# Performance work log

Measured on AMD Instinct MI355X. Metric: run time of the kernel, lower is better.

The kernel has to match this reference:

```python
import jax, jax.numpy as jnp
import numpy as np

N, D, K, MAX_ITER = 131072, 64, 512, 5


def setup_inputs() -> dict:
    key = jax.random.key(0)
    k1, k2, k3 = jax.random.split(key, 3)
    X = jax.random.normal(k1, (N, D), dtype=jnp.float32)
    centers = jax.random.normal(k2, (K, D), dtype=jnp.float32)
    repl_idx = jax.random.randint(k3, (MAX_ITER, K), 0, N, dtype=jnp.int32)
    return {"X": X, "centers": centers, "repl_idx": repl_idx}


def _assign(X, centers):
    # squared euclidean distance matrix [N, K]; argmin identical to cdist argmin
    x2 = jnp.sum(X * X, axis=1, keepdims=True)          # [N,1]
    c2 = jnp.sum(centers * centers, axis=1)             # [K]
    d2 = x2 + c2[None, :] - 2.0 * (X @ centers.T)       # [N,K]
    return jnp.argmin(d2, axis=1)


def reference(X, centers, repl_idx):
    n_clusters = centers.shape[0]
    assignments = None
    for i in range(MAX_ITER):
        assignments = _assign(X, centers)
        # scatter_mean: per-cluster sum / count (empty clusters -> 0, as torch_scatter)
        sums = jax.ops.segment_sum(X, assignments, num_segments=n_clusters)
        counts = jax.ops.segment_sum(jnp.ones((X.shape[0],), X.dtype), assignments,
                                     num_segments=n_clusters)
        new_centers = sums / jnp.maximum(counts, 1.0)[:, None]
        # re-initialize any exactly-zero entries from random data points
        new_centers_init = X[repl_idx[i]]                 # [K,D]
        new_centers = jnp.where(new_centers == 0, new_centers_init, new_centers)
        centers = new_centers
    return assignments, centers
```

## Files before the change

kernel.cpp:

```cpp
#include <hip/hip_runtime.h>

#define N_PTS 131072
#define KC    512
#define DIM   64
#define MAXIT 5
#define NCHUNK 64
#define CHUNK_PTS (N_PTS / NCHUNK)
#define FIXSCALE 1099511627776.0

typedef short v8s __attribute__((ext_vector_type(8)));
typedef float v4f __attribute__((ext_vector_type(4)));

__device__ __forceinline__ unsigned short bf16_rtne(float x) {
    unsigned int u = __float_as_uint(x);
    return (unsigned short)((u + 0x7FFFu + ((u >> 16) & 1u)) >> 16);
}
__device__ __forceinline__ float bf16_f32(unsigned short b) {
    return __uint_as_float(((unsigned int)b) << 16);
}
__device__ __forceinline__ void split3(float x, short& h, short& m, short& l) {
    unsigned short hb = bf16_rtne(x);
    float r1 = x - bf16_f32(hb);
    unsigned short mb = bf16_rtne(r1);
    float r2 = r1 - bf16_f32(mb);
    h = (short)hb; m = (short)mb; l = (short)bf16_rtne(r2);
}

__global__ __launch_bounds__(256) void prep_kernel(
        const float* __restrict__ C, float* __restrict__ c2out,
        unsigned short* __restrict__ Ch, unsigned short* __restrict__ Cm,
        unsigned short* __restrict__ Cl) {
    int k = blockIdx.x * 256 + threadIdx.x;
    if (k < KC) {
        float sq[DIM];
        #pragma unroll
        for (int j = 0; j < DIM; ++j) {
            float c = C[k * DIM + j];
            sq[j] = c * c;
            short h, m, l;
            split3(c, h, m, l);
            Ch[k * DIM + j] = (unsigned short)h;
            Cm[k * DIM + j] = (unsigned short)m;
            Cl[k * DIM + j] = (unsigned short)l;
        }
        #pragma unroll
        for (int st = 1; st < DIM; st <<= 1)
            #pragma unroll
            for (int j = 0; j < DIM; j += 2 * st)
                sq[j] = sq[j] + sq[j + st];
        c2out[k] = sq[0];
    }
}

__global__ __launch_bounds__(256, 4) void assign_kernel(
        const float* __restrict__ X,
        const unsigned short* __restrict__ Ch,
        const unsigned short* __restrict__ Cm,
        const unsigned short* __restrict__ Cl,
        const float* __restrict__ c2v, float* __restrict__ out_f) {
    __shared__ short Bt[6 * 64 * 8];
    __shared__ float c2t[KC];
    __shared__ float x2p[4][2][16][8];
    __shared__ float x2f[4][2][16];

    const int t   = threadIdx.x;
    const int wv  = t >> 6;
    const int l   = t & 63;
    const int row = l & 15;
    const int q   = l >> 4;
    const int pbase = blockIdx.x * 128 + wv * 32;

    for (int i = t; i < KC; i += 256) c2t[i] = c2v[i];

    v8s ah[2][2], am[2][2], al[2][2];
    #pragma unroll
    for (int T = 0; T < 2; ++T) {
        const float* xr = X + (size_t)(pbase + T * 16 + row) * DIM + q * 8;
        #pragma unroll
        for (int kc = 0; kc < 2; ++kc) {
            float4 v0 = *(const float4*)(xr + kc * 32);
            float4 v1 = *(const float4*)(xr + kc * 32 + 4);
            float e[8] = { v0.x, v0.y, v0.z, v0.w, v1.x, v1.y, v1.z, v1.w };
            v8s H, M, L;
            #pragma unroll
            for (int j = 0; j < 8; ++j) {
                short hh, mm, ll;
                split3(e[j], hh, mm, ll);
                H[j] = hh; M[j] = mm; L[j] = ll;
            }
            ah[T][kc] = H; am[T][kc] = M; al[T][kc] = L;
            float s0 = e[0]*e[0], s1 = e[1]*e[1], s2 = e[2]*e[2], s3 = e[3]*e[3];
            float s4 = e[4]*e[4], s5 = e[5]*e[5], s6 = e[6]*e[6], s7 = e[7]*e[7];
            x2p[wv][T][row][kc * 4 + q] =
                ((s0 + s1) + (s2 + s3)) + ((s4 + s5) + (s6 + s7));
        }
    }
    __syncthreads();
    if (t < 128) {
        int w2 = t >> 5, T2 = (t >> 4) & 1, pt = t & 15;
        const float* P = x2p[w2][T2][pt];
        x2f[w2][T2][pt] = ((P[0] + P[1]) + (P[2] + P[3]))
                        + ((P[4] + P[5]) + (P[6] + P[7]));
    }
    __syncthreads();
    float x2x[2][4];
    #pragma unroll
    for (int T = 0; T < 2; ++T)
        #pragma unroll
        for (int r = 0; r < 4; ++r)
            x2x[T][r] = x2f[wv][T][q * 4 + r];

    float bd[2][4];
    int   bk[2][4];
    #pragma unroll
    for (int T = 0; T < 2; ++T)
        #pragma unroll
        for (int r = 0; r < 4; ++r) { bd[T][r] = 3.4e38f; bk[T][r] = 0; }

    const unsigned short* const bases[3] = { Ch, Cm, Cl };
    #define CHUNK_GPTR(c, ct) ((const v8s*)(bases[(c) >> 7] +                 \
        ((size_t)((ct) * 16 + (((c) & 63) & 15)) * 64 +                       \
         (((c) >> 6) & 1) * 32 + (((c) & 63) >> 4) * 8)))

    v8s r1 = *CHUNK_GPTR(t, 0);
    v8s r2;
    if (t < 128) r2 = *CHUNK_GPTR(256 + t, 0);

    v8s* const BtV = (v8s*)Bt;
    for (int ct = 0; ct < 32; ++ct) {
        __syncthreads();
        BtV[t] = r1;
        if (t < 128) BtV[256 + t] = r2;
        if (ct < 31) {
            r1 = *CHUNK_GPTR(t, ct + 1);
            if (t < 128) r2 = *CHUNK_GPTR(256 + t, ct + 1);
        }
        __syncthreads();

        v8s bh0 = BtV[0 * 64 + l];
        v8s bh1 = BtV[1 * 64 + l];
        v8s bm0 = BtV[2 * 64 + l];
        v8s bm1 = BtV[3 * 64 + l];
        v8s bl0 = BtV[4 * 64 + l];
        v8s bl1 = BtV[5 * 64 + l];
        float c2k = c2t[ct * 16 + row];

        #pragma unroll
        for (int T = 0; T < 2; ++T) {
            v4f acc = {0.f, 0.f, 0.f, 0.f};
            acc = __builtin_amdgcn_mfma_f32_16x16x32_bf16(ah[T][0], bh0, acc, 0, 0, 0);
            acc = __builtin_amdgcn_mfma_f32_16x16x32_bf16(ah[T][1], bh1, acc, 0, 0, 0);
            acc = __builtin_amdgcn_mfma_f32_16x16x32_bf16(am[T][0], bh0, acc, 0, 0, 0);
            acc = __builtin_amdgcn_mfma_f32_16x16x32_bf16(am[T][1], bh1, acc, 0, 0, 0);
            acc = __builtin_amdgcn_mfma_f32_16x16x32_bf16(ah[T][0], bm0, acc, 0, 0, 0);
            acc = __builtin_amdgcn_mfma_f32_16x16x32_bf16(ah[T][1], bm1, acc, 0, 0, 0);
            acc = __builtin_amdgcn_mfma_f32_16x16x32_bf16(am[T][0], bm0, acc, 0, 0, 0);
            acc = __builtin_amdgcn_mfma_f32_16x16x32_bf16(am[T][1], bm1, acc, 0, 0, 0);
            acc = __builtin_amdgcn_mfma_f32_16x16x32_bf16(al[T][0], bh0, acc, 0, 0, 0);
            acc = __builtin_amdgcn_mfma_f32_16x16x32_bf16(al[T][1], bh1, acc, 0, 0, 0);
            acc = __builtin_amdgcn_mfma_f32_16x16x32_bf16(ah[T][0], bl0, acc, 0, 0, 0);
            acc = __builtin_amdgcn_mfma_f32_16x16x32_bf16(ah[T][1], bl1, acc, 0, 0, 0);
            #pragma unroll
            for (int r = 0; r < 4; ++r) {
                float tt = x2x[T][r] + c2k;
                float d2 = fmaf(-2.0f, acc[r], tt);
                if (d2 < bd[T][r]) { bd[T][r] = d2; bk[T][r] = ct * 16 + row; }
            }
        }
    }
    #undef CHUNK_GPTR

    #pragma unroll
    for (int T = 0; T < 2; ++T)
        #pragma unroll
        for (int r = 0; r < 4; ++r) {
            unsigned int b = __float_as_uint(bd[T][r]);
            b = (b & 0x80000000u) ? ~b : (b | 0x80000000u);
            unsigned long long key = ((unsigned long long)b << 32)
                                   | (unsigned int)bk[T][r];
            #pragma unroll
            for (int st = 1; st <= 8; st <<= 1) {
                unsigned long long o = __shfl_xor(key, st, 64);
                if (o < key) key = o;
            }
            if (row == 0) {
                int p = pbase + T * 16 + q * 4 + r;
                out_f[p] = (float)((int)(unsigned int)key);
            }
        }
}

__global__ __launch_bounds__(256) void accum_kernel(
        const float* __restrict__ X, const float* __restrict__ af,
        unsigned long long* __restrict__ qsums, int* __restrict__ counts) {
    __shared__ unsigned long long lsum[KC * 16];
    __shared__ int lcnt[KC];
    int slice = blockIdx.x & 3;
    int chunk = blockIdx.x >> 2;
    int p4 = threadIdx.x >> 2;
    int c4 = threadIdx.x & 3;

    for (int i = threadIdx.x; i < KC * 16; i += 256) lsum[i] = 0ull;
    for (int i = threadIdx.x; i < KC; i += 256) lcnt[i] = 0;
    __syncthreads();

    int base = chunk * CHUNK_PTS;
    #pragma unroll 2
    for (int it = 0; it < CHUNK_PTS / 64; ++it) {
        int n = base + it * 64 + p4;
        int a = (int)af[n];
        float4 xv = *(const float4*)(X + (size_t)n * DIM + slice * 16 + c4 * 4);
        long long q0 = (long long)llrint((double)xv.x * FIXSCALE);
        long long q1 = (long long)llrint((double)xv.y * FIXSCALE);
        long long q2 = (long long)llrint((double)xv.z * FIXSCALE);
        long long q3 = (long long)llrint((double)xv.w * FIXSCALE);
        atomicAdd(&lsum[a * 16 + c4 * 4 + 0], (unsigned long long)q0);
        atomicAdd(&lsum[a * 16 + c4 * 4 + 1], (unsigned long long)q1);
        atomicAdd(&lsum[a * 16 + c4 * 4 + 2], (unsigned long long)q2);
        atomicAdd(&lsum[a * 16 + c4 * 4 + 3], (unsigned long long)q3);
        if (slice == 0 && c4 == 0) atomicAdd(&lcnt[a], 1);
    }
    __syncthreads();

    for (int i = threadIdx.x; i < KC * 16; i += 256) {
        unsigned long long v = lsum[i];
        if (v != 0ull)
            atomicAdd(&qsums[(i >> 4) * DIM + slice * 16 + (i & 15)], v);
    }
    if (slice == 0)
        for (int i = threadIdx.x; i < KC; i += 256) {
            int v = lcnt[i];
            if (v != 0) atomicAdd(&counts[i], v);
        }
}

__global__ __launch_bounds__(256) void update_kernel(
        const unsigned long long* __restrict__ qsums,
        const int* __restrict__ counts,
        const int* __restrict__ repl, const float* __restrict__ X,
        float* __restrict__ outC, float* __restrict__ c2v,
        unsigned short* __restrict__ Ch, unsigned short* __restrict__ Cm,
        unsigned short* __restrict__ Cl) {
    int k = blockIdx.x * 4 + (threadIdx.x >> 6);
    int d = threadIdx.x & 63;

    long long qq = (long long)qsums[k * DIM + d];
    float s = (float)((double)qq * (1.0 / FIXSCALE));
    float cnt = (float)counts[k];
    float v = s / fmaxf(cnt, 1.0f);
    if (v == 0.0f) v = X[(size_t)repl[k] * DIM + d];
    outC[k * DIM + d] = v;

    short h, m, l;
    split3(v, h, m, l);
    Ch[k * DIM + d] = (unsigned short)h;
    Cm[k * DIM + d] = (unsigned short)m;
    Cl[k * DIM + d] = (unsigned short)l;

    float sq = v * v;
    #pragma unroll
    for (int st = 1; st < 64; st <<= 1)
        sq += __shfl_xor(sq, st, 64);
    if (d == 0) c2v[k] = sq;
}

extern "C" void kernel_launch(void* const* d_in, const int* in_sizes, int n_in,
                              void* d_out, int out_size, void* d_ws, size_t ws_size,
                              hipStream_t stream) {
    const float* X    = (const float*)d_in[0];
    const float* C0   = (const float*)d_in[1];
    const int*   repl = (const int*)d_in[2];
    float* out = (float*)d_out;

    char* ws = (char*)d_ws;
    unsigned short* Ch = (unsigned short*)(ws + 0);
    unsigned short* Cm = (unsigned short*)(ws + (64 << 10));
    unsigned short* Cl = (unsigned short*)(ws + (128 << 10));
    unsigned long long* qsums = (unsigned long long*)(ws + (192 << 10));
    int*   counts = (int*)  (ws + (448 << 10));
    float* c2v    = (float*)(ws + (450 << 10));

    prep_kernel<<<2, 256, 0, stream>>>(C0, c2v, Ch, Cm, Cl);

    for (int i = 0; i < MAXIT; ++i) {
        assign_kernel<<<N_PTS / 128, 256, 0, stream>>>(
            X, Ch, Cm, Cl, c2v, out);

        hipMemsetAsync(qsums, 0, KC * DIM * sizeof(unsigned long long)
                                 + KC * sizeof(int), stream);

        accum_kernel<<<NCHUNK * 4, 256, 0, stream>>>(X, out, qsums, counts);

        update_kernel<<<KC / 4, 256, 0, stream>>>(
            qsums, counts, repl + i * KC, X, out + N_PTS, c2v, Ch, Cm, Cl);
    }
}
```

Measured before the change: 474.6 us.

## Stage 64 centers per sync in assign, drop memset, widen accum blocks

The assign kernel now stages 64 centers (all three bf16 planes) into shared memory per barrier pair instead of 16, which cuts the number of barriers and global prefetch rounds. The trade is a larger LDS tile, more prefetch registers and an occupancy hint lowered from 4 to 3 blocks. The per-iteration hipMemsetAsync is removed: prep zeroes the sums and counts once, and update_kernel clears them after reading. accum_kernel now runs 1024-thread blocks so each block's shared-memory histogram serves more threads.

```diff
diff --git a/kernel.cpp b/kernel.cpp
--- a/kernel.cpp
+++ b/kernel.cpp
@@ -29,7 +29,8 @@
 __global__ __launch_bounds__(256) void prep_kernel(
         const float* __restrict__ C, float* __restrict__ c2out,
         unsigned short* __restrict__ Ch, unsigned short* __restrict__ Cm,
-        unsigned short* __restrict__ Cl) {
+        unsigned short* __restrict__ Cl,
+        unsigned long long* __restrict__ qsums, int* __restrict__ counts) {
     int k = blockIdx.x * 256 + threadIdx.x;
     if (k < KC) {
         float sq[DIM];
@@ -50,15 +51,18 @@
                 sq[j] = sq[j] + sq[j + st];
         c2out[k] = sq[0];
     }
-}
-
-__global__ __launch_bounds__(256, 4) void assign_kernel(
+    int t = blockIdx.x * 256 + threadIdx.x;
+    for (int i = t; i < KC * DIM; i += 512) qsums[i] = 0ull;
+    if (t < KC) counts[t] = 0;
+}
+
+__global__ __launch_bounds__(256, 3) void assign_kernel(
         const float* __restrict__ X,
         const unsigned short* __restrict__ Ch,
         const unsigned short* __restrict__ Cm,
         const unsigned short* __restrict__ Cl,
         const float* __restrict__ c2v, float* __restrict__ out_f) {
-    __shared__ short Bt[6 * 64 * 8];
+    __shared__ short Bt[1536 * 8];
     __shared__ float c2t[KC];
     __shared__ float x2p[4][2][16][8];
     __shared__ float x2f[4][2][16];
@@ -118,53 +122,57 @@
         for (int r = 0; r < 4; ++r) { bd[T][r] = 3.4e38f; bk[T][r] = 0; }
 
     const unsigned short* const bases[3] = { Ch, Cm, Cl };
-    #define CHUNK_GPTR(c, ct) ((const v8s*)(bases[(c) >> 7] +                 \
-        ((size_t)((ct) * 16 + (((c) & 63) & 15)) * 64 +                       \
-         (((c) >> 6) & 1) * 32 + (((c) & 63) >> 4) * 8)))
-
-    v8s r1 = *CHUNK_GPTR(t, 0);
-    v8s r2;
-    if (t < 128) r2 = *CHUNK_GPTR(256 + t, 0);
+    #define CHUNK_GPTR(c, s) ((const v8s*)(bases[((c) % 384) >> 7] +          \
+        ((size_t)((s) * 64 + ((c) / 384) * 16 + ((c) & 15)) * 64 +            \
+         ((((c) % 384) >> 6) & 1) * 32 + (((c) & 63) >> 4) * 8)))
+
+    v8s rr[6];
+    #pragma unroll
+    for (int r = 0; r < 6; ++r) rr[r] = *CHUNK_GPTR(t + 256 * r, 0);
 
     v8s* const BtV = (v8s*)Bt;
-    for (int ct = 0; ct < 32; ++ct) {
+    for (int s = 0; s < 8; ++s) {
         __syncthreads();
-        BtV[t] = r1;
-        if (t < 128) BtV[256 + t] = r2;
-        if (ct < 31) {
-            r1 = *CHUNK_GPTR(t, ct + 1);
-            if (t < 128) r2 = *CHUNK_GPTR(256 + t, ct + 1);
+        #pragma unroll
+        for (int r = 0; r < 6; ++r) BtV[t + 256 * r] = rr[r];
+        if (s < 7) {
+            #pragma unroll
+            for (int r = 0; r < 6; ++r) rr[r] = *CHUNK_GPTR(t + 256 * r, s + 1);
         }
         __syncthreads();
 
-        v8s bh0 = BtV[0 * 64 + l];
-        v8s bh1 = BtV[1 * 64 + l];
-        v8s bm0 = BtV[2 * 64 + l];
-        v8s bm1 = BtV[3 * 64 + l];
-        v8s bl0 = BtV[4 * 64 + l];
-        v8s bl1 = BtV[5 * 64 + l];
-        float c2k = c2t[ct * 16 + row];
-
-        #pragma unroll
-        for (int T = 0; T < 2; ++T) {
-            v4f acc = {0.f, 0.f, 0.f, 0.f};
-            acc = __builtin_amdgcn_mfma_f32_16x16x32_bf16(ah[T][0], bh0, acc, 0, 0, 0);
-            acc = __builtin_amdgcn_mfma_f32_16x16x32_bf16(ah[T][1], bh1, acc, 0, 0, 0);
-            acc = __builtin_amdgcn_mfma_f32_16x16x32_bf16(am[T][0], bh0, acc, 0, 0, 0);
-            acc = __builtin_amdgcn_mfma_f32_16x16x32_bf16(am[T][1], bh1, acc, 0, 0, 0);
-            acc = __builtin_amdgcn_mfma_f32_16x16x32_bf16(ah[T][0], bm0, acc, 0, 0, 0);
-            acc = __builtin_amdgcn_mfma_f32_16x16x32_bf16(ah[T][1], bm1, acc, 0, 0, 0);
-            acc = __builtin_amdgcn_mfma_f32_16x16x32_bf16(am[T][0], bm0, acc, 0, 0, 0);
-            acc = __builtin_amdgcn_mfma_f32_16x16x32_bf16(am[T][1], bm1, acc, 0, 0, 0);
-            acc = __builtin_amdgcn_mfma_f32_16x16x32_bf16(al[T][0], bh0, acc, 0, 0, 0);
-            acc = __builtin_amdgcn_mfma_f32_16x16x32_bf16(al[T][1], bh1, acc, 0, 0, 0);
-            acc = __builtin_amdgcn_mfma_f32_16x16x32_bf16(ah[T][0], bl0, acc, 0, 0, 0);
-            acc = __builtin_amdgcn_mfma_f32_16x16x32_bf16(ah[T][1], bl1, acc, 0, 0, 0);
-            #pragma unroll
-            for (int r = 0; r < 4; ++r) {
-                float tt = x2x[T][r] + c2k;
-                float d2 = fmaf(-2.0f, acc[r], tt);
-                if (d2 < bd[T][r]) { bd[T][r] = d2; bk[T][r] = ct * 16 + row; }
+        #pragma unroll
+        for (int sub = 0; sub < 4; ++sub) {
+            v8s bh0 = BtV[sub * 384 + 0 * 64 + l];
+            v8s bh1 = BtV[sub * 384 + 1 * 64 + l];
+            v8s bm0 = BtV[sub * 384 + 2 * 64 + l];
+            v8s bm1 = BtV[sub * 384 + 3 * 64 + l];
+            v8s bl0 = BtV[sub * 384 + 4 * 64 + l];
+            v8s bl1 = BtV[sub * 384 + 5 * 64 + l];
+            float c2k = c2t[s * 64 + sub * 16 + row];
+            int   kk  = s * 64 + sub * 16 + row;
+
+            #pragma unroll
+            for (int T = 0; T < 2; ++T) {
+                v4f acc = {0.f, 0.f, 0.f, 0.f};
+                acc = __builtin_amdgcn_mfma_f32_16x16x32_bf16(ah[T][0], bh0, acc, 0, 0, 0);
+                acc = __builtin_amdgcn_mfma_f32_16x16x32_bf16(ah[T][1], bh1, acc, 0, 0, 0);
+                acc = __builtin_amdgcn_mfma_f32_16x16x32_bf16(am[T][0], bh0, acc, 0, 0, 0);
+                acc = __builtin_amdgcn_mfma_f32_16x16x32_bf16(am[T][1], bh1, acc, 0, 0, 0);
+                acc = __builtin_amdgcn_mfma_f32_16x16x32_bf16(ah[T][0], bm0, acc, 0, 0, 0);
+                acc = __builtin_amdgcn_mfma_f32_16x16x32_bf16(ah[T][1], bm1, acc, 0, 0, 0);
+                acc = __builtin_amdgcn_mfma_f32_16x16x32_bf16(am[T][0], bm0, acc, 0, 0, 0);
+                acc = __builtin_amdgcn_mfma_f32_16x16x32_bf16(am[T][1], bm1, acc, 0, 0, 0);
+                acc = __builtin_amdgcn_mfma_f32_16x16x32_bf16(al[T][0], bh0, acc, 0, 0, 0);
+                acc = __builtin_amdgcn_mfma_f32_16x16x32_bf16(al[T][1], bh1, acc, 0, 0, 0);
+                acc = __builtin_amdgcn_mfma_f32_16x16x32_bf16(ah[T][0], bl0, acc, 0, 0, 0);
+                acc = __builtin_amdgcn_mfma_f32_16x16x32_bf16(ah[T][1], bl1, acc, 0, 0, 0);
+                #pragma unroll
+                for (int r = 0; r < 4; ++r) {
+                    float tt = x2x[T][r] + c2k;
+                    float d2 = fmaf(-2.0f, acc[r], tt);
+                    if (d2 < bd[T][r]) { bd[T][r] = d2; bk[T][r] = kk; }
+                }
             }
         }
     }
@@ -190,7 +198,7 @@
         }
 }
 
-__global__ __launch_bounds__(256) void accum_kernel(
+__global__ __launch_bounds__(1024) void accum_kernel(
         const float* __restrict__ X, const float* __restrict__ af,
         unsigned long long* __restrict__ qsums, int* __restrict__ counts) {
     __shared__ unsigned long long lsum[KC * 16];
@@ -200,14 +208,14 @@
     int p4 = threadIdx.x >> 2;
     int c4 = threadIdx.x & 3;
 
-    for (int i = threadIdx.x; i < KC * 16; i += 256) lsum[i] = 0ull;
-    for (int i = threadIdx.x; i < KC; i += 256) lcnt[i] = 0;
+    for (int i = threadIdx.x; i < KC * 16; i += 1024) lsum[i] = 0ull;
+    if (threadIdx.x < KC) lcnt[threadIdx.x] = 0;
     __syncthreads();
 
     int base = chunk * CHUNK_PTS;
     #pragma unroll 2
-    for (int it = 0; it < CHUNK_PTS / 64; ++it) {
-        int n = base + it * 64 + p4;
+    for (int it = 0; it < CHUNK_PTS / 256; ++it) {
+        int n = base + it * 256 + p4;
         int a = (int)af[n];
         float4 xv = *(const float4*)(X + (size_t)n * DIM + slice * 16 + c4 * 4);
         long long q0 = (long long)llrint((double)xv.x * FIXSCALE);
@@ -222,40 +230,43 @@
     }
     __syncthreads();
 
-    for (int i = threadIdx.x; i < KC * 16; i += 256) {
+    for (int i = threadIdx.x; i < KC * 16; i += 1024) {
         unsigned long long v = lsum[i];
         if (v != 0ull)
             atomicAdd(&qsums[(i >> 4) * DIM + slice * 16 + (i & 15)], v);
     }
-    if (slice == 0)
-        for (int i = threadIdx.x; i < KC; i += 256) {
-            int v = lcnt[i];
-            if (v != 0) atomicAdd(&counts[i], v);
-        }
+    if (slice == 0 && threadIdx.x < KC) {
+        int v = lcnt[threadIdx.x];
+        if (v != 0) atomicAdd(&counts[threadIdx.x], v);
+    }
 }
 
 __global__ __launch_bounds__(256) void update_kernel(
-        const unsigned long long* __restrict__ qsums,
-        const int* __restrict__ counts,
+        unsigned long long* __restrict__ qsums,
+        int* __restrict__ counts,
         const int* __restrict__ repl, const float* __restrict__ X,
         float* __restrict__ outC, float* __restrict__ c2v,
         unsigned short* __restrict__ Ch, unsigned short* __restrict__ Cm,
         unsigned short* __restrict__ Cl) {
     int k = blockIdx.x * 4 + (threadIdx.x >> 6);
     int d = threadIdx.x & 63;
-
-    long long qq = (long long)qsums[k * DIM + d];
+    int idx = k * DIM + d;
+
+    long long qq = (long long)qsums[idx];
+    float cnt = (float)counts[k];
+    qsums[idx] = 0ull;
+    if (d == 0) counts[k] = 0;
+
     float s = (float)((double)qq * (1.0 / FIXSCALE));
-    float cnt = (float)counts[k];
     float v = s / fmaxf(cnt, 1.0f);
     if (v == 0.0f) v = X[(size_t)repl[k] * DIM + d];
-    outC[k * DIM + d] = v;
+    outC[idx] = v;
 
     short h, m, l;
     split3(v, h, m, l);
-    Ch[k * DIM + d] = (unsigned short)h;
-    Cm[k * DIM + d] = (unsigned short)m;
-    Cl[k * DIM + d] = (unsigned short)l;
+    Ch[idx] = (unsigned short)h;
+    Cm[idx] = (unsigned short)m;
+    Cl[idx] = (unsigned short)l;
 
     float sq = v * v;
     #pragma unroll
@@ -280,16 +291,13 @@
     int*   counts = (int*)  (ws + (448 << 10));
     float* c2v    = (float*)(ws + (450 << 10));
 
-    prep_kernel<<<2, 256, 0, stream>>>(C0, c2v, Ch, Cm, Cl);
+    prep_kernel<<<2, 256, 0, stream>>>(C0, c2v, Ch, Cm, Cl, qsums, counts);
 
     for (int i = 0; i < MAXIT; ++i) {
         assign_kernel<<<N_PTS / 128, 256, 0, stream>>>(
             X, Ch, Cm, Cl, c2v, out);
 
-        hipMemsetAsync(qsums, 0, KC * DIM * sizeof(unsigned long long)
-                                 + KC * sizeof(int), stream);
-
-        accum_kernel<<<NCHUNK * 4, 256, 0, stream>>>(X, out, qsums, counts);
+        accum_kernel<<<NCHUNK * 4, 1024, 0, stream>>>(X, out, qsums, counts);
 
         update_kernel<<<KC / 4, 256, 0, stream>>>(
             qsums, counts, repl + i * KC, X, out + N_PTS, c2v, Ch, Cm, Cl);
```

Result: slower. 515.6 us (+8.6%).
